# Kernel tuning notes

Hardware: AMD Instinct MI355X
Metric: run time of the kernel (lower is better)

## Reference

```python
import jax, jax.numpy as jnp
import numpy as np

N_NODES = 100000
N_EDGES = 1600000
N_GRAPHS = 512
NODE_DIM = 64   # len(node_indices)
GRAPH_DIM = 16  # len(graph_indices) == graph_channels
HIDDEN = 128
OUT = 8


def setup_inputs() -> dict:
    key = jax.random.key(0)
    ks = jax.random.split(key, 12)
    x = jax.random.normal(ks[0], (N_NODES, NODE_DIM + GRAPH_DIM), dtype=jnp.float32)
    edge_index = jax.random.randint(ks[1], (2, N_EDGES), 0, N_NODES, dtype=jnp.int64)
    batch = jnp.sort(jax.random.randint(ks[2], (N_NODES,), 0, N_GRAPHS, dtype=jnp.int64))
    def lin(k, fan_in, fan_out):
        lim = 1.0 / np.sqrt(fan_in)
        return jax.random.uniform(k, (fan_in, fan_out), jnp.float32, -lim, lim)
    return {
        "x": x, "edge_index": edge_index, "batch": batch,
        "W1": lin(ks[3], NODE_DIM, HIDDEN), "b1": jnp.zeros((HIDDEN,), jnp.float32),
        "W2": lin(ks[4], HIDDEN, HIDDEN),   "b2": jnp.zeros((HIDDEN,), jnp.float32),
        "Wm1": lin(ks[5], HIDDEN + GRAPH_DIM, HIDDEN), "bm1": jnp.zeros((HIDDEN,), jnp.float32),
        "Wm2": lin(ks[6], HIDDEN, OUT), "bm2": jnp.zeros((OUT,), jnp.float32),
    }


def _gcn_conv(h_in, src, dst, W, b):
    # PyG GCNConv: h = X W; out = D^{-1/2}(A+I)D^{-1/2} h + b, deg over A+I.
    h = h_in @ W                                        # [N, H]
    deg = jnp.zeros((N_NODES,), h.dtype).at[dst].add(1.0) + 1.0  # +1 self loop
    dinv = jax.lax.rsqrt(deg)                           # [N]
    norm = dinv[src] * dinv[dst]                        # [E]
    out = jnp.zeros_like(h).at[dst].add(norm[:, None] * h[src])
    out = out + (dinv * dinv)[:, None] * h              # self-loop term
    return out + b


def _mean_pool(v, batch):
    cnt = jax.ops.segment_sum(jnp.ones((v.shape[0],), v.dtype), batch, num_segments=N_GRAPHS)
    s = jax.ops.segment_sum(v, batch, num_segments=N_GRAPHS)
    return s / jnp.maximum(cnt, 1.0)[:, None]


def reference(x, edge_index, batch, W1, b1, W2, b2, Wm1, bm1, Wm2, bm2):
    src, dst = edge_index[0], edge_index[1]
    node_t = x[:, :NODE_DIM]                 # node_indices slice
    graph_t = _mean_pool(x[:, NODE_DIM:], batch)  # graph_indices slice, pooled [G, 16]
    h = _gcn_conv(node_t, src, dst, W1, b1)
    h = jax.nn.relu(h)                       # dropout is identity in eval mode
    h = _gcn_conv(h, src, dst, W2, b2)
    g = _mean_pool(h, batch)                 # [G, H]
    g = jnp.concatenate([g, graph_t], axis=1)
    g = jax.nn.relu(g @ Wm1 + bm1)
    return g @ Wm2 + bm2                     # [G, OUT]
```

## Files before the change

### kernel.cpp

```cpp
#include <hip/hip_runtime.h>
#include <hip/hip_bf16.h>

#define N_NODES 100000
#define N_EDGES 1600000
#define N_GRAPHS 512
#define NODE_DIM 64
#define GRAPH_DIM 16
#define HIDDEN 128
#define OUT_DIM 8

#define NBUCKETS 391
#define BIN_CAP 8192
#define EPB 4096

__device__ __forceinline__ float bflo(unsigned u) { return __uint_as_float(u << 16); }
__device__ __forceinline__ float bfhi(unsigned u) { return __uint_as_float(u & 0xffff0000u); }


__global__ __launch_bounds__(256) void k_binplace(const int* __restrict__ src,
                                                  const int* __restrict__ dst,
                                                  int* __restrict__ gcur,
                                                  unsigned* __restrict__ bin) {
    __shared__ int cnt[NBUCKETS];
    __shared__ int base[NBUCKETS];
    int t = threadIdx.x;
    for (int i = t; i < NBUCKETS; i += 256) cnt[i] = 0;
    __syncthreads();
    int e0 = blockIdx.x * EPB;
#pragma unroll
    for (int k = 0; k < EPB / 256; k++) {
        int e = e0 + k * 256 + t;
        if (e < N_EDGES) atomicAdd(&cnt[dst[e] >> 8], 1);
    }
    __syncthreads();
    for (int i = t; i < NBUCKETS; i += 256) {
        int c = cnt[i];
        base[i] = (c > 0) ? atomicAdd(&gcur[i], c) : 0;
        cnt[i] = 0;
    }
    __syncthreads();
#pragma unroll
    for (int k = 0; k < EPB / 256; k++) {
        int e = e0 + k * 256 + t;
        if (e < N_EDGES) {
            int d = dst[e];
            int b = d >> 8;
            int p = atomicAdd(&cnt[b], 1);
            bin[(size_t)b * BIN_CAP + base[b] + p] = ((unsigned)src[e] << 8) | (unsigned)(d & 255);
        }
    }
}


__global__ __launch_bounds__(256) void k_degBf(const int* __restrict__ gcur,
                                               const unsigned* __restrict__ bin,
                                               int* __restrict__ degcnt,
                                               float* __restrict__ dinv,
                                               int* __restrict__ bsum) {
    __shared__ int cnt[256];
    int b = blockIdx.x, t = threadIdx.x;
    cnt[t] = 0;
    __syncthreads();
    int n = gcur[b];
    const unsigned* seg = bin + (size_t)b * BIN_CAP;
    for (int i = t; i < n; i += 256) atomicAdd(&cnt[seg[i] & 255u], 1);
    __syncthreads();
    int c = cnt[t];
    int node = b * 256 + t;
    if (node < N_NODES) {
        degcnt[node] = c;
        dinv[node] = rsqrtf((float)c + 1.0f);
    }
    __syncthreads();
    for (int o = 128; o > 0; o >>= 1) {
        if (t < o) cnt[t] += cnt[t + o];
        __syncthreads();
    }
    if (t == 0) bsum[b] = cnt[0];
}


__global__ __launch_bounds__(512) void k_scanb(const int* __restrict__ bsum,
                                               int* __restrict__ bofs) {
    __shared__ int s[512];
    int t = threadIdx.x;
    int v = (t < NBUCKETS) ? bsum[t] : 0;
    s[t] = v;
    __syncthreads();
    for (int o = 1; o < 512; o <<= 1) {
        int u = (t >= o) ? s[t - o] : 0;
        __syncthreads();
        s[t] += u;
        __syncthreads();
    }
    if (t < NBUCKETS) bofs[t] = s[t] - v;
}


__global__ __launch_bounds__(256) void k_rowfill(const int* __restrict__ degcnt,
                                                 const int* __restrict__ bofs,
                                                 const int* __restrict__ gcur,
                                                 const unsigned* __restrict__ bin,
                                                 const float* __restrict__ dinv,
                                                 int* __restrict__ row_start,
                                                 int2* __restrict__ csre,
                                                 float* __restrict__ gt_sum) {
    __shared__ int sc[256];
    __shared__ int rsl[256];
    __shared__ int cnt[256];
    __shared__ float dl[256];
    int b = blockIdx.x, t = threadIdx.x;
    if (b < 32) gt_sum[b * 256 + t] = 0.0f;
    int node = b * 256 + t;
    int v = (node < N_NODES) ? degcnt[node] : 0;
    sc[t] = v;
    __syncthreads();
    for (int o = 1; o < 256; o <<= 1) {
        int u = (t >= o) ? sc[t - o] : 0;
        __syncthreads();
        sc[t] += u;
        __syncthreads();
    }
    int rs = bofs[b] + sc[t] - v;
    if (node < N_NODES) row_start[node] = rs;
    rsl[t] = rs;
    cnt[t] = 0;
    dl[t] = rsqrtf((float)v + 1.0f);
    __syncthreads();
    int n = gcur[b];
    const unsigned* seg = bin + (size_t)b * BIN_CAP;
    for (int i = t; i < n; i += 256) {
        unsigned e = seg[i];
        int dlidx = (int)(e & 255u);
        int s = (int)(e >> 8);
        int pos = rsl[dlidx] + atomicAdd(&cnt[dlidx], 1);
        csre[pos] = make_int2(s, __float_as_int(dinv[s] * dl[dlidx]));
    }
}


__global__ __launch_bounds__(256) void k_packstat(const float* __restrict__ x,
                                                  const int* __restrict__ batch,
                                                  ushort* __restrict__ xb,
                                                  float* __restrict__ gt_sum) {
    int t = threadIdx.x;
    int i0 = blockIdx.x * 64;
    for (int idx = t; idx < 64 * 32; idx += 256) {
        int node = i0 + (idx >> 5);
        if (node < N_NODES) {
            int c2 = idx & 31;
            float2 v = *(const float2*)&x[(size_t)node * 80 + c2 * 2];
            __hip_bfloat16 lo = __float2bfloat16(v.x);
            __hip_bfloat16 hi = __float2bfloat16(v.y);
            ushort2 pv = make_ushort2(*(ushort*)&lo, *(ushort*)&hi);
            ((ushort2*)xb)[(size_t)node * 32 + c2] = pv;
        }
    }
    int c = t & 15, sub = t >> 4;
    int iend = min(i0 + 64, N_NODES);
    float acc = 0.0f;
    int g = -1;
    for (int i = i0 + sub; i < iend; i += 16) {
        int bi = batch[i];
        if (bi != g) {
            if (g >= 0) atomicAdd(&gt_sum[g * GRAPH_DIM + c], acc);
            acc = 0.0f; g = bi;
        }
        acc += x[(size_t)i * 80 + NODE_DIM + c];
    }
    if (g >= 0) atomicAdd(&gt_sum[g * GRAPH_DIM + c], acc);
}


#define LDX(s_) __uint_as_float((unsigned)xb[(size_t)(s_)*64 + lane] << 16)

__global__ __launch_bounds__(256) void k_conv1(const int2* __restrict__ csre,
                                               const int* __restrict__ row_start,
                                               const float* __restrict__ dinv,
                                               const ushort* __restrict__ xb,
                                               const float* __restrict__ W,
                                               const float* __restrict__ bias,
                                               ushort* __restrict__ C,
                                               float* __restrict__ gsum2) {
    __shared__ float zs[8][64];
    int t = threadIdx.x;
    if (blockIdx.x < 256) gsum2[blockIdx.x * 256 + t] = 0.0f;
    int w = t >> 6, lane = t & 63;
    int nA = blockIdx.x * 8 + w * 2;
    int nB = nA + 1;
    int rsA = row_start[nA], reA = (nA == N_NODES - 1) ? N_EDGES : row_start[nA + 1];
    int rsB = row_start[nB], reB = (nB == N_NODES - 1) ? N_EDGES : row_start[nB + 1];
    float aA0 = 0.f, aA1 = 0.f, aA2 = 0.f, aA3 = 0.f;
    float aB0 = 0.f, aB1 = 0.f, aB2 = 0.f, aB3 = 0.f;
    int kA = rsA, kB = rsB;
    while (kA + 4 <= reA && kB + 4 <= reB) {
        int2 eA0 = csre[kA], eA1 = csre[kA + 1], eA2 = csre[kA + 2], eA3 = csre[kA + 3];
        int2 eB0 = csre[kB], eB1 = csre[kB + 1], eB2 = csre[kB + 2], eB3 = csre[kB + 3];
        float vA0 = LDX(eA0.x), vA1 = LDX(eA1.x), vA2 = LDX(eA2.x), vA3 = LDX(eA3.x);
        float vB0 = LDX(eB0.x), vB1 = LDX(eB1.x), vB2 = LDX(eB2.x), vB3 = LDX(eB3.x);
        aA0 += __int_as_float(eA0.y) * vA0; aA1 += __int_as_float(eA1.y) * vA1;
        aA2 += __int_as_float(eA2.y) * vA2; aA3 += __int_as_float(eA3.y) * vA3;
        aB0 += __int_as_float(eB0.y) * vB0; aB1 += __int_as_float(eB1.y) * vB1;
        aB2 += __int_as_float(eB2.y) * vB2; aB3 += __int_as_float(eB3.y) * vB3;
        kA += 4; kB += 4;
    }
    while (kA + 4 <= reA) {
        int2 e0 = csre[kA], e1 = csre[kA + 1], e2 = csre[kA + 2], e3 = csre[kA + 3];
        float v0 = LDX(e0.x), v1 = LDX(e1.x), v2 = LDX(e2.x), v3 = LDX(e3.x);
        aA0 += __int_as_float(e0.y) * v0; aA1 += __int_as_float(e1.y) * v1;
        aA2 += __int_as_float(e2.y) * v2; aA3 += __int_as_float(e3.y) * v3;
        kA += 4;
    }
    while (kB + 4 <= reB) {
        int2 e0 = csre[kB], e1 = csre[kB + 1], e2 = csre[kB + 2], e3 = csre[kB + 3];
        float v0 = LDX(e0.x), v1 = LDX(e1.x), v2 = LDX(e2.x), v3 = LDX(e3.x);
        aB0 += __int_as_float(e0.y) * v0; aB1 += __int_as_float(e1.y) * v1;
        aB2 += __int_as_float(e2.y) * v2; aB3 += __int_as_float(e3.y) * v3;
        kB += 4;
    }
    while (kA < reA && kB < reB) {
        int2 eA = csre[kA]; int2 eB = csre[kB];
        aA0 += __int_as_float(eA.y) * LDX(eA.x);
        aB0 += __int_as_float(eB.y) * LDX(eB.x);
        kA++; kB++;
    }
    while (kA < reA) { int2 e = csre[kA]; aA0 += __int_as_float(e.y) * LDX(e.x); kA++; }
    while (kB < reB) { int2 e = csre[kB]; aB0 += __int_as_float(e.y) * LDX(e.x); kB++; }
    float dA = dinv[nA], dB = dinv[nB];
    zs[w * 2][lane]     = aA0 + aA1 + aA2 + aA3 + dA * dA * LDX(nA);
    zs[w * 2 + 1][lane] = aB0 + aB1 + aB2 + aB3 + dB * dB * LDX(nB);
    __syncthreads();
    if (t < 128) {
        int j = t;
        float acc[8];
#pragma unroll
        for (int m = 0; m < 8; m++) acc[m] = 0.0f;
        for (int k = 0; k < 64; k++) {
            float wv = W[k * 128 + j];
#pragma unroll
            for (int m = 0; m < 8; m++) acc[m] += zs[m][k] * wv;
        }
        float b = bias[j];
        size_t row0 = (size_t)blockIdx.x * 8;
#pragma unroll
        for (int m = 0; m < 8; m++) {
            float v = fmaxf(acc[m] + b, 0.0f);
            __hip_bfloat16 hv = __float2bfloat16(v);
            C[(row0 + m) * 128 + j] = *(ushort*)&hv;
        }
    }
}


__global__ __launch_bounds__(256) void k_gather2(const int2* __restrict__ csre,
                                                 const int* __restrict__ row_start,
                                                 const float* __restrict__ dinv,
                                                 const unsigned* __restrict__ h,
                                                 const int* __restrict__ batch,
                                                 float* __restrict__ gsum2) {
    __shared__ float2 red[8][64];
    int w = threadIdx.x >> 6, lane = threadIdx.x & 63;
    int nA = blockIdx.x * 8 + w * 2;
    int nB = nA + 1;
    int rsA = row_start[nA], reA = (nA == N_NODES - 1) ? N_EDGES : row_start[nA + 1];
    int rsB = row_start[nB], reB = (nB == N_NODES - 1) ? N_EDGES : row_start[nB + 1];
    float2 aA0 = {0.f,0.f}, aA1 = {0.f,0.f}, aA2 = {0.f,0.f}, aA3 = {0.f,0.f};
    float2 aB0 = {0.f,0.f}, aB1 = {0.f,0.f}, aB2 = {0.f,0.f}, aB3 = {0.f,0.f};
    int kA = rsA, kB = rsB;
#define FMA2(acc_, wbits_, u_) { float w_ = __int_as_float(wbits_); \
                             acc_.x += w_ * bflo(u_); acc_.y += w_ * bfhi(u_); }
    while (kA + 4 <= reA && kB + 4 <= reB) {
        int2 eA0 = csre[kA], eA1 = csre[kA + 1], eA2 = csre[kA + 2], eA3 = csre[kA + 3];
        int2 eB0 = csre[kB], eB1 = csre[kB + 1], eB2 = csre[kB + 2], eB3 = csre[kB + 3];
        unsigned uA0 = h[(size_t)eA0.x * 64 + lane], uA1 = h[(size_t)eA1.x * 64 + lane];
        unsigned uA2 = h[(size_t)eA2.x * 64 + lane], uA3 = h[(size_t)eA3.x * 64 + lane];
        unsigned uB0 = h[(size_t)eB0.x * 64 + lane], uB1 = h[(size_t)eB1.x * 64 + lane];
        unsigned uB2 = h[(size_t)eB2.x * 64 + lane], uB3 = h[(size_t)eB3.x * 64 + lane];
        FMA2(aA0, eA0.y, uA0); FMA2(aA1, eA1.y, uA1); FMA2(aA2, eA2.y, uA2); FMA2(aA3, eA3.y, uA3);
        FMA2(aB0, eB0.y, uB0); FMA2(aB1, eB1.y, uB1); FMA2(aB2, eB2.y, uB2); FMA2(aB3, eB3.y, uB3);
        kA += 4; kB += 4;
    }
    while (kA + 4 <= reA) {
        int2 e0 = csre[kA], e1 = csre[kA + 1], e2 = csre[kA + 2], e3 = csre[kA + 3];
        unsigned u0 = h[(size_t)e0.x * 64 + lane], u1 = h[(size_t)e1.x * 64 + lane];
        unsigned u2 = h[(size_t)e2.x * 64 + lane], u3 = h[(size_t)e3.x * 64 + lane];
        FMA2(aA0, e0.y, u0); FMA2(aA1, e1.y, u1); FMA2(aA2, e2.y, u2); FMA2(aA3, e3.y, u3);
        kA += 4;
    }
    while (kB + 4 <= reB) {
        int2 e0 = csre[kB], e1 = csre[kB + 1], e2 = csre[kB + 2], e3 = csre[kB + 3];
        unsigned u0 = h[(size_t)e0.x * 64 + lane], u1 = h[(size_t)e1.x * 64 + lane];
        unsigned u2 = h[(size_t)e2.x * 64 + lane], u3 = h[(size_t)e3.x * 64 + lane];
        FMA2(aB0, e0.y, u0); FMA2(aB1, e1.y, u1); FMA2(aB2, e2.y, u2); FMA2(aB3, e3.y, u3);
        kB += 4;
    }
    while (kA < reA && kB < reB) {
        int2 eA = csre[kA]; int2 eB = csre[kB];
        unsigned uA = h[(size_t)eA.x * 64 + lane], uB = h[(size_t)eB.x * 64 + lane];
        FMA2(aA0, eA.y, uA); FMA2(aB0, eB.y, uB);
        kA++; kB++;
    }
    while (kA < reA) {
        int2 e = csre[kA]; unsigned u = h[(size_t)e.x * 64 + lane];
        FMA2(aA0, e.y, u); kA++;
    }
    while (kB < reB) {
        int2 e = csre[kB]; unsigned u = h[(size_t)e.x * 64 + lane];
        FMA2(aB0, e.y, u); kB++;
    }
#undef FMA2
    float dA = dinv[nA], dB = dinv[nB];
    unsigned usA = h[(size_t)nA * 64 + lane];
    unsigned usB = h[(size_t)nB * 64 + lane];
    float2 rA, rB;
    rA.x = aA0.x + aA1.x + aA2.x + aA3.x + dA * dA * bflo(usA);
    rA.y = aA0.y + aA1.y + aA2.y + aA3.y + dA * dA * bfhi(usA);
    rB.x = aB0.x + aB1.x + aB2.x + aB3.x + dB * dB * bflo(usB);
    rB.y = aB0.y + aB1.y + aB2.y + aB3.y + dB * dB * bfhi(usB);
    red[w * 2][lane] = rA;
    red[w * 2 + 1][lane] = rB;
    __syncthreads();
    int g0 = batch[blockIdx.x * 8];
    int g7 = batch[blockIdx.x * 8 + 7];
    if (g0 == g7) {
        if (w == 0) {
            float sx = 0.f, sy = 0.f;
#pragma unroll
            for (int q = 0; q < 8; q++) { sx += red[q][lane].x; sy += red[q][lane].y; }
            atomicAdd(&gsum2[g0 * 128 + 2 * lane], sx);
            atomicAdd(&gsum2[g0 * 128 + 2 * lane + 1], sy);
        }
    } else {
        int gA = batch[nA], gB = batch[nB];
        atomicAdd(&gsum2[gA * 128 + 2 * lane], rA.x);
        atomicAdd(&gsum2[gA * 128 + 2 * lane + 1], rA.y);
        atomicAdd(&gsum2[gB * 128 + 2 * lane], rB.x);
        atomicAdd(&gsum2[gB * 128 + 2 * lane + 1], rB.y);
    }
}


__global__ __launch_bounds__(128) void k_mlp(const float* __restrict__ gsum2,
                                             const float* __restrict__ gt_sum,
                                             const int* __restrict__ batch,
                                             const float* __restrict__ W2,
                                             const float* __restrict__ b2,
                                             const float* __restrict__ Wm1,
                                             const float* __restrict__ bm1,
                                             const float* __restrict__ Wm2,
                                             const float* __restrict__ bm2,
                                             float* __restrict__ out) {
    __shared__ float srow[HIDDEN];
    __shared__ float g144[HIDDEN + GRAPH_DIM];
    __shared__ float sm[HIDDEN];
    __shared__ int cnt_sh;
    int b = blockIdx.x;
    int j = threadIdx.x;
    float raw = gsum2[b * 128 + j];
    float gtraw = (j < GRAPH_DIM) ? gt_sum[b * GRAPH_DIM + j] : 0.0f;
    if (j == 0) {
        int lo = 0, hi = N_NODES;
        while (lo < hi) { int m = (lo + hi) >> 1; if (batch[m] < b) lo = m + 1; else hi = m; }
        int a = lo;
        lo = 0; hi = N_NODES;
        while (lo < hi) { int m = (lo + hi) >> 1; if (batch[m] < b + 1) lo = m + 1; else hi = m; }
        cnt_sh = lo - a;
    }
    __syncthreads();
    float inv = 1.0f / fmaxf((float)cnt_sh, 1.0f);
    srow[j] = raw * inv;
    if (j < GRAPH_DIM) g144[128 + j] = gtraw * inv;
    __syncthreads();
    float z = b2[j];
    for (int k = 0; k < 128; k++) z += srow[k] * W2[k * 128 + j];
    g144[j] = z;
    __syncthreads();
    float acc = bm1[j];
    for (int k = 0; k < HIDDEN + GRAPH_DIM; k++) acc += g144[k] * Wm1[k * 128 + j];
    sm[j] = fmaxf(acc, 0.0f);
    __syncthreads();
    if (j < OUT_DIM) {
        float o = bm2[j];
        for (int k = 0; k < 128; k++) o += sm[k] * Wm2[k * OUT_DIM + j];
        out[b * OUT_DIM + j] = o;
    }
}

extern "C" void kernel_launch(void* const* d_in, const int* in_sizes, int n_in,
                              void* d_out, int out_size, void* d_ws, size_t ws_size,
                              hipStream_t stream) {
    const float* x    = (const float*)d_in[0];
    const int*   edge = (const int*)d_in[1];
    const int*   src  = edge;
    const int*   dst  = edge + N_EDGES;
    const int*   batch= (const int*)d_in[2];
    const float* W1   = (const float*)d_in[3];
    const float* b1   = (const float*)d_in[4];
    const float* W2   = (const float*)d_in[5];
    const float* b2   = (const float*)d_in[6];
    const float* Wm1  = (const float*)d_in[7];
    const float* bm1  = (const float*)d_in[8];
    const float* Wm2  = (const float*)d_in[9];
    const float* bm2  = (const float*)d_in[10];
    float* out = (float*)d_out;

    char* ws = (char*)d_ws;
    char* p = ws;
    unsigned* bin   = (unsigned*)p;  p += (size_t)NBUCKETS * BIN_CAP * 4;
    int2*  csre     = (int2*)p;      p += (size_t)N_EDGES * 8;
    ushort* h1b     = (ushort*)p;    p += (size_t)N_NODES * 128 * 2;
    ushort* xb      = (ushort*)p;    p += (size_t)N_NODES * 64 * 2;
    int*   degcnt   = (int*)p;       p += (size_t)NBUCKETS * 256 * 4;
    int*   row_start= (int*)p;       p += (size_t)N_NODES * 4;
    float* dinv     = (float*)p;     p += (size_t)N_NODES * 4;
    int*   gcur     = (int*)p;       p += (size_t)NBUCKETS * 4;
    int*   bsum     = (int*)p;       p += 512 * 4;
    int*   bofs     = (int*)p;       p += 512 * 4;
    float* gt_sum   = (float*)p;     p += (size_t)N_GRAPHS * GRAPH_DIM * 4;
    float* gsum2    = (float*)p;     p += (size_t)N_GRAPHS * 128 * 4;

    hipMemsetAsync(gcur, 0, (size_t)NBUCKETS * 4, stream);

    k_binplace<<<(N_EDGES + EPB - 1) / EPB, 256, 0, stream>>>(src, dst, gcur, bin);
    k_degBf<<<NBUCKETS, 256, 0, stream>>>(gcur, bin, degcnt, dinv, bsum);
    k_scanb<<<1, 512, 0, stream>>>(bsum, bofs);
    k_rowfill<<<NBUCKETS, 256, 0, stream>>>(degcnt, bofs, gcur, bin, dinv, row_start, csre, gt_sum);

    k_packstat<<<(N_NODES + 63) / 64, 256, 0, stream>>>(x, batch, xb, gt_sum);

    k_conv1<<<N_NODES / 8, 256, 0, stream>>>(csre, row_start, dinv, xb, W1, b1, h1b, gsum2);

    k_gather2<<<N_NODES / 8, 256, 0, stream>>>(csre, row_start, dinv,
                                               (const unsigned*)h1b, batch, gsum2);

    k_mlp<<<N_GRAPHS, 128, 0, stream>>>(gsum2, gt_sum, batch, W2, b2, Wm1, bm1, Wm2, bm2, out);
}
```

Measured before the change: 248.2 us.

## Halve bucket size, fuse bucket scan into degree kernel, pad CSR for unrolled gathers

Buckets now hold 128 destination nodes instead of 256, which doubles the number of blocks used for binning, degree counting and row fill. The separate bucket-sum scan kernel is removed: block 0 of the degree kernel scans the global bucket counts directly. The CSR gets padding entries and a sentinel row_start, so both gather kernels can run a single 8-wide unrolled loop with masked weights instead of several remainder loops. This cuts one launch and the tail-loop branching, at the cost of some wasted loads on short rows. Block 0 reads gcur, which is final after the previous kernel, so the fused scan is correct.

```diff
diff --git a/kernel.cpp b/kernel.cpp
--- a/kernel.cpp
+++ b/kernel.cpp
@@ -9,8 +9,9 @@
 #define HIDDEN 128
 #define OUT_DIM 8
 
-#define NBUCKETS 391
-#define BIN_CAP 8192
+#define NBUCKETS 782
+#define BNODES 128
+#define BIN_CAP 4096
 #define EPB 4096
 
 __device__ __forceinline__ float bflo(unsigned u) { return __uint_as_float(u << 16); }
@@ -30,7 +31,7 @@
 #pragma unroll
     for (int k = 0; k < EPB / 256; k++) {
         int e = e0 + k * 256 + t;
-        if (e < N_EDGES) atomicAdd(&cnt[dst[e] >> 8], 1);
+        if (e < N_EDGES) atomicAdd(&cnt[dst[e] >> 7], 1);
     }
     __syncthreads();
     for (int i = t; i < NBUCKETS; i += 256) {
@@ -44,56 +45,55 @@
         int e = e0 + k * 256 + t;
         if (e < N_EDGES) {
             int d = dst[e];
-            int b = d >> 8;
+            int b = d >> 7;
             int p = atomicAdd(&cnt[b], 1);
-            bin[(size_t)b * BIN_CAP + base[b] + p] = ((unsigned)src[e] << 8) | (unsigned)(d & 255);
-        }
-    }
-}
-
-
-__global__ __launch_bounds__(256) void k_degBf(const int* __restrict__ gcur,
-                                               const unsigned* __restrict__ bin,
-                                               int* __restrict__ degcnt,
-                                               float* __restrict__ dinv,
-                                               int* __restrict__ bsum) {
-    __shared__ int cnt[256];
+            bin[(size_t)b * BIN_CAP + base[b] + p] = ((unsigned)src[e] << 7) | (unsigned)(d & 127);
+        }
+    }
+}
+
+
+__global__ __launch_bounds__(256) void k_degscan(const int* __restrict__ gcur,
+                                                 const unsigned* __restrict__ bin,
+                                                 int* __restrict__ degcnt,
+                                                 float* __restrict__ dinv,
+                                                 int* __restrict__ bofs) {
+    __shared__ int cnt[BNODES];
     int b = blockIdx.x, t = threadIdx.x;
-    cnt[t] = 0;
+    if (t < BNODES) cnt[t] = 0;
     __syncthreads();
     int n = gcur[b];
     const unsigned* seg = bin + (size_t)b * BIN_CAP;
-    for (int i = t; i < n; i += 256) atomicAdd(&cnt[seg[i] & 255u], 1);
-    __syncthreads();
-    int c = cnt[t];
-    int node = b * 256 + t;
-    if (node < N_NODES) {
+    for (int i = t; i < n; i += 256) atomicAdd(&cnt[seg[i] & 127u], 1);
+    __syncthreads();
+    int node = b * BNODES + t;
+    if (t < BNODES && node < N_NODES) {
+        int c = cnt[t];
         degcnt[node] = c;
         dinv[node] = rsqrtf((float)c + 1.0f);
     }
-    __syncthreads();
-    for (int o = 128; o > 0; o >>= 1) {
-        if (t < o) cnt[t] += cnt[t + o];
+    if (b == 0) {
+        __shared__ int ls[256];
+        int i0 = 4 * t;
+        int c0 = (i0 + 0 < NBUCKETS) ? gcur[i0 + 0] : 0;
+        int c1 = (i0 + 1 < NBUCKETS) ? gcur[i0 + 1] : 0;
+        int c2 = (i0 + 2 < NBUCKETS) ? gcur[i0 + 2] : 0;
+        int c3 = (i0 + 3 < NBUCKETS) ? gcur[i0 + 3] : 0;
+        int s = c0 + c1 + c2 + c3;
+        ls[t] = s;
         __syncthreads();
-    }
-    if (t == 0) bsum[b] = cnt[0];
-}
-
-
-__global__ __launch_bounds__(512) void k_scanb(const int* __restrict__ bsum,
-                                               int* __restrict__ bofs) {
-    __shared__ int s[512];
-    int t = threadIdx.x;
-    int v = (t < NBUCKETS) ? bsum[t] : 0;
-    s[t] = v;
-    __syncthreads();
-    for (int o = 1; o < 512; o <<= 1) {
-        int u = (t >= o) ? s[t - o] : 0;
-        __syncthreads();
-        s[t] += u;
-        __syncthreads();
-    }
-    if (t < NBUCKETS) bofs[t] = s[t] - v;
+        for (int o = 1; o < 256; o <<= 1) {
+            int u = (t >= o) ? ls[t - o] : 0;
+            __syncthreads();
+            ls[t] += u;
+            __syncthreads();
+        }
+        int run = ls[t] - s;
+        if (i0 + 0 < NBUCKETS) bofs[i0 + 0] = run; run += c0;
+        if (i0 + 1 < NBUCKETS) bofs[i0 + 1] = run; run += c1;
+        if (i0 + 2 < NBUCKETS) bofs[i0 + 2] = run; run += c2;
+        if (i0 + 3 < NBUCKETS) bofs[i0 + 3] = run;
+    }
 }
 
 
@@ -105,36 +105,46 @@
                                                  int* __restrict__ row_start,
                                                  int2* __restrict__ csre,
                                                  float* __restrict__ gt_sum) {
-    __shared__ int sc[256];
-    __shared__ int rsl[256];
-    __shared__ int cnt[256];
-    __shared__ float dl[256];
+    __shared__ int sc[BNODES];
+    __shared__ int rsl[BNODES];
+    __shared__ int cnt[BNODES];
+    __shared__ float dl[BNODES];
     int b = blockIdx.x, t = threadIdx.x;
     if (b < 32) gt_sum[b * 256 + t] = 0.0f;
-    int node = b * 256 + t;
-    int v = (node < N_NODES) ? degcnt[node] : 0;
-    sc[t] = v;
-    __syncthreads();
-    for (int o = 1; o < 256; o <<= 1) {
-        int u = (t >= o) ? sc[t - o] : 0;
+    int node = b * BNODES + t;
+    int v = 0;
+    if (t < BNODES) {
+        v = (node < N_NODES) ? degcnt[node] : 0;
+        sc[t] = v;
+    }
+    __syncthreads();
+    for (int o = 1; o < BNODES; o <<= 1) {
+        int u = 0;
+        if (t < BNODES && t >= o) u = sc[t - o];
         __syncthreads();
-        sc[t] += u;
+        if (t < BNODES) sc[t] += u;
         __syncthreads();
     }
-    int rs = bofs[b] + sc[t] - v;
-    if (node < N_NODES) row_start[node] = rs;
-    rsl[t] = rs;
-    cnt[t] = 0;
-    dl[t] = rsqrtf((float)v + 1.0f);
+    if (t < BNODES) {
+        int rs = bofs[b] + sc[t] - v;
+        if (node < N_NODES) row_start[node] = rs;
+        rsl[t] = rs;
+        cnt[t] = 0;
+        dl[t] = rsqrtf((float)v + 1.0f);
+    }
     __syncthreads();
     int n = gcur[b];
     const unsigned* seg = bin + (size_t)b * BIN_CAP;
     for (int i = t; i < n; i += 256) {
         unsigned e = seg[i];
-        int dlidx = (int)(e & 255u);
-        int s = (int)(e >> 8);
+        int dlidx = (int)(e & 127u);
+        int s = (int)(e >> 7);
         int pos = rsl[dlidx] + atomicAdd(&cnt[dlidx], 1);
         csre[pos] = make_int2(s, __float_as_int(dinv[s] * dl[dlidx]));
+    }
+    if (b == NBUCKETS - 1) {
+        if (t < 8) csre[N_EDGES + t] = make_int2(0, 0);
+        if (t == 8) row_start[N_NODES] = N_EDGES;
     }
 }
 
@@ -185,50 +195,52 @@
     __shared__ float zs[8][64];
     int t = threadIdx.x;
     if (blockIdx.x < 256) gsum2[blockIdx.x * 256 + t] = 0.0f;
-    int w = t >> 6, lane = t & 63;
-    int nA = blockIdx.x * 8 + w * 2;
+    int wv = t >> 6, lane = t & 63;
+    int nA = blockIdx.x * 8 + wv * 2;
     int nB = nA + 1;
-    int rsA = row_start[nA], reA = (nA == N_NODES - 1) ? N_EDGES : row_start[nA + 1];
-    int rsB = row_start[nB], reB = (nB == N_NODES - 1) ? N_EDGES : row_start[nB + 1];
+    int kA = row_start[nA], reA = row_start[nA + 1];
+    int kB = reA,           reB = row_start[nB + 1];
     float aA0 = 0.f, aA1 = 0.f, aA2 = 0.f, aA3 = 0.f;
     float aB0 = 0.f, aB1 = 0.f, aB2 = 0.f, aB3 = 0.f;
-    int kA = rsA, kB = rsB;
-    while (kA + 4 <= reA && kB + 4 <= reB) {
-        int2 eA0 = csre[kA], eA1 = csre[kA + 1], eA2 = csre[kA + 2], eA3 = csre[kA + 3];
-        int2 eB0 = csre[kB], eB1 = csre[kB + 1], eB2 = csre[kB + 2], eB3 = csre[kB + 3];
-        float vA0 = LDX(eA0.x), vA1 = LDX(eA1.x), vA2 = LDX(eA2.x), vA3 = LDX(eA3.x);
-        float vB0 = LDX(eB0.x), vB1 = LDX(eB1.x), vB2 = LDX(eB2.x), vB3 = LDX(eB3.x);
-        aA0 += __int_as_float(eA0.y) * vA0; aA1 += __int_as_float(eA1.y) * vA1;
-        aA2 += __int_as_float(eA2.y) * vA2; aA3 += __int_as_float(eA3.y) * vA3;
-        aB0 += __int_as_float(eB0.y) * vB0; aB1 += __int_as_float(eB1.y) * vB1;
-        aB2 += __int_as_float(eB2.y) * vB2; aB3 += __int_as_float(eB3.y) * vB3;
-        kA += 4; kB += 4;
-    }
-    while (kA + 4 <= reA) {
-        int2 e0 = csre[kA], e1 = csre[kA + 1], e2 = csre[kA + 2], e3 = csre[kA + 3];
-        float v0 = LDX(e0.x), v1 = LDX(e1.x), v2 = LDX(e2.x), v3 = LDX(e3.x);
-        aA0 += __int_as_float(e0.y) * v0; aA1 += __int_as_float(e1.y) * v1;
-        aA2 += __int_as_float(e2.y) * v2; aA3 += __int_as_float(e3.y) * v3;
-        kA += 4;
-    }
-    while (kB + 4 <= reB) {
-        int2 e0 = csre[kB], e1 = csre[kB + 1], e2 = csre[kB + 2], e3 = csre[kB + 3];
-        float v0 = LDX(e0.x), v1 = LDX(e1.x), v2 = LDX(e2.x), v3 = LDX(e3.x);
-        aB0 += __int_as_float(e0.y) * v0; aB1 += __int_as_float(e1.y) * v1;
-        aB2 += __int_as_float(e2.y) * v2; aB3 += __int_as_float(e3.y) * v3;
-        kB += 4;
-    }
-    while (kA < reA && kB < reB) {
-        int2 eA = csre[kA]; int2 eB = csre[kB];
-        aA0 += __int_as_float(eA.y) * LDX(eA.x);
-        aB0 += __int_as_float(eB.y) * LDX(eB.x);
-        kA++; kB++;
-    }
-    while (kA < reA) { int2 e = csre[kA]; aA0 += __int_as_float(e.y) * LDX(e.x); kA++; }
-    while (kB < reB) { int2 e = csre[kB]; aB0 += __int_as_float(e.y) * LDX(e.x); kB++; }
+    while (kA < reA || kB < reB) {
+        if (kA < reA) {
+            int2 e0 = csre[kA],     e1 = csre[kA + 1], e2 = csre[kA + 2], e3 = csre[kA + 3];
+            int2 e4 = csre[kA + 4], e5 = csre[kA + 5], e6 = csre[kA + 6], e7 = csre[kA + 7];
+            float w0 = (kA + 0 < reA) ? __int_as_float(e0.y) : 0.f;
+            float w1 = (kA + 1 < reA) ? __int_as_float(e1.y) : 0.f;
+            float w2 = (kA + 2 < reA) ? __int_as_float(e2.y) : 0.f;
+            float w3 = (kA + 3 < reA) ? __int_as_float(e3.y) : 0.f;
+            float w4 = (kA + 4 < reA) ? __int_as_float(e4.y) : 0.f;
+            float w5 = (kA + 5 < reA) ? __int_as_float(e5.y) : 0.f;
+            float w6 = (kA + 6 < reA) ? __int_as_float(e6.y) : 0.f;
+            float w7 = (kA + 7 < reA) ? __int_as_float(e7.y) : 0.f;
+            float v0 = LDX(e0.x), v1 = LDX(e1.x), v2 = LDX(e2.x), v3 = LDX(e3.x);
+            float v4 = LDX(e4.x), v5 = LDX(e5.x), v6 = LDX(e6.x), v7 = LDX(e7.x);
+            aA0 += w0 * v0; aA1 += w1 * v1; aA2 += w2 * v2; aA3 += w3 * v3;
+            aA0 += w4 * v4; aA1 += w5 * v5; aA2 += w6 * v6; aA3 += w7 * v7;
+            kA += 8;
+        }
+        if (kB < reB) {
+            int2 e0 = csre[kB],     e1 = csre[kB + 1], e2 = csre[kB + 2], e3 = csre[kB + 3];
+            int2 e4 = csre[kB + 4], e5 = csre[kB + 5], e6 = csre[kB + 6], e7 = csre[kB + 7];
+            float w0 = (kB + 0 < reB) ? __int_as_float(e0.y) : 0.f;
+            float w1 = (kB + 1 < reB) ? __int_as_float(e1.y) : 0.f;
+            float w2 = (kB + 2 < reB) ? __int_as_float(e2.y) : 0.f;
+            float w3 = (kB + 3 < reB) ? __int_as_float(e3.y) : 0.f;
+            float w4 = (kB + 4 < reB) ? __int_as_float(e4.y) : 0.f;
+            float w5 = (kB + 5 < reB) ? __int_as_float(e5.y) : 0.f;
+            float w6 = (kB + 6 < reB) ? __int_as_float(e6.y) : 0.f;
+            float w7 = (kB + 7 < reB) ? __int_as_float(e7.y) : 0.f;
+            float v0 = LDX(e0.x), v1 = LDX(e1.x), v2 = LDX(e2.x), v3 = LDX(e3.x);
+            float v4 = LDX(e4.x), v5 = LDX(e5.x), v6 = LDX(e6.x), v7 = LDX(e7.x);
+            aB0 += w0 * v0; aB1 += w1 * v1; aB2 += w2 * v2; aB3 += w3 * v3;
+            aB0 += w4 * v4; aB1 += w5 * v5; aB2 += w6 * v6; aB3 += w7 * v7;
+            kB += 8;
+        }
+    }
     float dA = dinv[nA], dB = dinv[nB];
-    zs[w * 2][lane]     = aA0 + aA1 + aA2 + aA3 + dA * dA * LDX(nA);
-    zs[w * 2 + 1][lane] = aB0 + aB1 + aB2 + aB3 + dB * dB * LDX(nB);
+    zs[wv * 2][lane]     = aA0 + aA1 + aA2 + aA3 + dA * dA * LDX(nA);
+    zs[wv * 2 + 1][lane] = aB0 + aB1 + aB2 + aB3 + dB * dB * LDX(nB);
     __syncthreads();
     if (t < 128) {
         int j = t;
@@ -236,9 +248,9 @@
 #pragma unroll
         for (int m = 0; m < 8; m++) acc[m] = 0.0f;
         for (int k = 0; k < 64; k++) {
-            float wv = W[k * 128 + j];
-#pragma unroll
-            for (int m = 0; m < 8; m++) acc[m] += zs[m][k] * wv;
+            float wv2 = W[k * 128 + j];
+#pragma unroll
+            for (int m = 0; m < 8; m++) acc[m] += zs[m][k] * wv2;
         }
         float b = bias[j];
         size_t row0 = (size_t)blockIdx.x * 8;
@@ -262,51 +274,50 @@
     int w = threadIdx.x >> 6, lane = threadIdx.x & 63;
     int nA = blockIdx.x * 8 + w * 2;
     int nB = nA + 1;
-    int rsA = row_start[nA], reA = (nA == N_NODES - 1) ? N_EDGES : row_start[nA + 1];
-    int rsB = row_start[nB], reB = (nB == N_NODES - 1) ? N_EDGES : row_start[nB + 1];
+    int kA = row_start[nA], reA = row_start[nA + 1];
+    int kB = reA,           reB = row_start[nB + 1];
     float2 aA0 = {0.f,0.f}, aA1 = {0.f,0.f}, aA2 = {0.f,0.f}, aA3 = {0.f,0.f};
     float2 aB0 = {0.f,0.f}, aB1 = {0.f,0.f}, aB2 = {0.f,0.f}, aB3 = {0.f,0.f};
-    int kA = rsA, kB = rsB;
-#define FMA2(acc_, wbits_, u_) { float w_ = __int_as_float(wbits_); \
-                             acc_.x += w_ * bflo(u_); acc_.y += w_ * bfhi(u_); }
-    while (kA + 4 <= reA && kB + 4 <= reB) {
-        int2 eA0 = csre[kA], eA1 = csre[kA + 1], eA2 = csre[kA + 2], eA3 = csre[kA + 3];
-        int2 eB0 = csre[kB], eB1 = csre[kB + 1], eB2 = csre[kB + 2], eB3 = csre[kB + 3];
-        unsigned uA0 = h[(size_t)eA0.x * 64 + lane], uA1 = h[(size_t)eA1.x * 64 + lane];
-        unsigned uA2 = h[(size_t)eA2.x * 64 + lane], uA3 = h[(size_t)eA3.x * 64 + lane];
-        unsigned uB0 = h[(size_t)eB0.x * 64 + lane], uB1 = h[(size_t)eB1.x * 64 + lane];
-        unsigned uB2 = h[(size_t)eB2.x * 64 + lane], uB3 = h[(size_t)eB3.x * 64 + lane];
-        FMA2(aA0, eA0.y, uA0); FMA2(aA1, eA1.y, uA1); FMA2(aA2, eA2.y, uA2); FMA2(aA3, eA3.y, uA3);
-        FMA2(aB0, eB0.y, uB0); FMA2(aB1, eB1.y, uB1); FMA2(aB2, eB2.y, uB2); FMA2(aB3, eB3.y, uB3);
-        kA += 4; kB += 4;
-    }
-    while (kA + 4 <= reA) {
-        int2 e0 = csre[kA], e1 = csre[kA + 1], e2 = csre[kA + 2], e3 = csre[kA + 3];
-        unsigned u0 = h[(size_t)e0.x * 64 + lane], u1 = h[(size_t)e1.x * 64 + lane];
-        unsigned u2 = h[(size_t)e2.x * 64 + lane], u3 = h[(size_t)e3.x * 64 + lane];
-        FMA2(aA0, e0.y, u0); FMA2(aA1, e1.y, u1); FMA2(aA2, e2.y, u2); FMA2(aA3, e3.y, u3);
-        kA += 4;
-    }
-    while (kB + 4 <= reB) {
-        int2 e0 = csre[kB], e1 = csre[kB + 1], e2 = csre[kB + 2], e3 = csre[kB + 3];
-        unsigned u0 = h[(size_t)e0.x * 64 + lane], u1 = h[(size_t)e1.x * 64 + lane];
-        unsigned u2 = h[(size_t)e2.x * 64 + lane], u3 = h[(size_t)e3.x * 64 + lane];
-        FMA2(aB0, e0.y, u0); FMA2(aB1, e1.y, u1); FMA2(aB2, e2.y, u2); FMA2(aB3, e3.y, u3);
-        kB += 4;
-    }
-    while (kA < reA && kB < reB) {
-        int2 eA = csre[kA]; int2 eB = csre[kB];
-        unsigned uA = h[(size_t)eA.x * 64 + lane], uB = h[(size_t)eB.x * 64 + lane];
-        FMA2(aA0, eA.y, uA); FMA2(aB0, eB.y, uB);
-        kA++; kB++;
-    }
-    while (kA < reA) {
-        int2 e = csre[kA]; unsigned u = h[(size_t)e.x * 64 + lane];
-        FMA2(aA0, e.y, u); kA++;
-    }
-    while (kB < reB) {
-        int2 e = csre[kB]; unsigned u = h[(size_t)e.x * 64 + lane];
-        FMA2(aB0, e.y, u); kB++;
+#define FMA2(acc_, w_, u_) { acc_.x += (w_) * bflo(u_); acc_.y += (w_) * bfhi(u_); }
+    while (kA < reA || kB < reB) {
+        if (kA < reA) {
+            int2 e0 = csre[kA],     e1 = csre[kA + 1], e2 = csre[kA + 2], e3 = csre[kA + 3];
+            int2 e4 = csre[kA + 4], e5 = csre[kA + 5], e6 = csre[kA + 6], e7 = csre[kA + 7];
+            float w0 = (kA + 0 < reA) ? __int_as_float(e0.y) : 0.f;
+            float w1 = (kA + 1 < reA) ? __int_as_float(e1.y) : 0.f;
+            float w2 = (kA + 2 < reA) ? __int_as_float(e2.y) : 0.f;
+            float w3 = (kA + 3 < reA) ? __int_as_float(e3.y) : 0.f;
+            float w4 = (kA + 4 < reA) ? __int_as_float(e4.y) : 0.f;
+            float w5 = (kA + 5 < reA) ? __int_as_float(e5.y) : 0.f;
+            float w6 = (kA + 6 < reA) ? __int_as_float(e6.y) : 0.f;
+            float w7 = (kA + 7 < reA) ? __int_as_float(e7.y) : 0.f;
+            unsigned u0 = h[(size_t)e0.x * 64 + lane], u1 = h[(size_t)e1.x * 64 + lane];
+            unsigned u2 = h[(size_t)e2.x * 64 + lane], u3 = h[(size_t)e3.x * 64 + lane];
+            unsigned u4 = h[(size_t)e4.x * 64 + lane], u5 = h[(size_t)e5.x * 64 + lane];
+            unsigned u6 = h[(size_t)e6.x * 64 + lane], u7 = h[(size_t)e7.x * 64 + lane];
+            FMA2(aA0, w0, u0); FMA2(aA1, w1, u1); FMA2(aA2, w2, u2); FMA2(aA3, w3, u3);
+            FMA2(aA0, w4, u4); FMA2(aA1, w5, u5); FMA2(aA2, w6, u6); FMA2(aA3, w7, u7);
+            kA += 8;
+        }
+        if (kB < reB) {
+            int2 e0 = csre[kB],     e1 = csre[kB + 1], e2 = csre[kB + 2], e3 = csre[kB + 3];
+            int2 e4 = csre[kB + 4], e5 = csre[kB + 5], e6 = csre[kB + 6], e7 = csre[kB + 7];
+            float w0 = (kB + 0 < reB) ? __int_as_float(e0.y) : 0.f;
+            float w1 = (kB + 1 < reB) ? __int_as_float(e1.y) : 0.f;
+            float w2 = (kB + 2 < reB) ? __int_as_float(e2.y) : 0.f;
+            float w3 = (kB + 3 < reB) ? __int_as_float(e3.y) : 0.f;
+            float w4 = (kB + 4 < reB) ? __int_as_float(e4.y) : 0.f;
+            float w5 = (kB + 5 < reB) ? __int_as_float(e5.y) : 0.f;
+            float w6 = (kB + 6 < reB) ? __int_as_float(e6.y) : 0.f;
+            float w7 = (kB + 7 < reB) ? __int_as_float(e7.y) : 0.f;
+            unsigned u0 = h[(size_t)e0.x * 64 + lane], u1 = h[(size_t)e1.x * 64 + lane];
+            unsigned u2 = h[(size_t)e2.x * 64 + lane], u3 = h[(size_t)e3.x * 64 + lane];
+            unsigned u4 = h[(size_t)e4.x * 64 + lane], u5 = h[(size_t)e5.x * 64 + lane];
+            unsigned u6 = h[(size_t)e6.x * 64 + lane], u7 = h[(size_t)e7.x * 64 + lane];
+            FMA2(aB0, w0, u0); FMA2(aB1, w1, u1); FMA2(aB2, w2, u2); FMA2(aB3, w3, u3);
+            FMA2(aB0, w4, u4); FMA2(aB1, w5, u5); FMA2(aB2, w6, u6); FMA2(aB3, w7, u7);
+            kB += 8;
+        }
     }
 #undef FMA2
     float dA = dinv[nA], dB = dinv[nB];
@@ -407,23 +418,21 @@
     char* ws = (char*)d_ws;
     char* p = ws;
     unsigned* bin   = (unsigned*)p;  p += (size_t)NBUCKETS * BIN_CAP * 4;
-    int2*  csre     = (int2*)p;      p += (size_t)N_EDGES * 8;
+    int2*  csre     = (int2*)p;      p += ((size_t)N_EDGES + 8) * 8;
     ushort* h1b     = (ushort*)p;    p += (size_t)N_NODES * 128 * 2;
     ushort* xb      = (ushort*)p;    p += (size_t)N_NODES * 64 * 2;
-    int*   degcnt   = (int*)p;       p += (size_t)NBUCKETS * 256 * 4;
-    int*   row_start= (int*)p;       p += (size_t)N_NODES * 4;
+    int*   degcnt   = (int*)p;       p += (size_t)NBUCKETS * BNODES * 4;
+    int*   row_start= (int*)p;       p += ((size_t)N_NODES + 1) * 4;
     float* dinv     = (float*)p;     p += (size_t)N_NODES * 4;
     int*   gcur     = (int*)p;       p += (size_t)NBUCKETS * 4;
-    int*   bsum     = (int*)p;       p += 512 * 4;
-    int*   bofs     = (int*)p;       p += 512 * 4;
+    int*   bofs     = (int*)p;       p += (size_t)NBUCKETS * 4;
     float* gt_sum   = (float*)p;     p += (size_t)N_GRAPHS * GRAPH_DIM * 4;
     float* gsum2    = (float*)p;     p += (size_t)N_GRAPHS * 128 * 4;
 
     hipMemsetAsync(gcur, 0, (size_t)NBUCKETS * 4, stream);
 
     k_binplace<<<(N_EDGES + EPB - 1) / EPB, 256, 0, stream>>>(src, dst, gcur, bin);
-    k_degBf<<<NBUCKETS, 256, 0, stream>>>(gcur, bin, degcnt, dinv, bsum);
-    k_scanb<<<1, 512, 0, stream>>>(bsum, bofs);
+    k_degscan<<<NBUCKETS, 256, 0, stream>>>(gcur, bin, degcnt, dinv, bofs);
     k_rowfill<<<NBUCKETS, 256, 0, stream>>>(degcnt, bofs, gcur, bin, dinv, row_start, csre, gt_sum);
 
     k_packstat<<<(N_NODES + 63) / 64, 256, 0, stream>>>(x, batch, xb, gt_sum);
```

After: 290.5 us. 1.17x slower.

## Split hidden features into two channel planes and gather each plane separately

Applied to the files above, without the earlier changes.

conv1 now writes its 128-channel bf16 output as two planes of 64 channels, [N,64] each, instead of one interleaved [N,128] array. The second gather launches twice as many blocks, and each block aggregates one plane for 8 nodes, interleaving the two phases so that nearby blocks share a plane. The aim is to halve the bytes fetched per neighbour per lane and make the gathered working set smaller and more cache-friendly. The cost is reading the CSR edge lists twice and issuing twice as many blocks and atomics per channel group. It also reuses row end A as row start B, which assumes consecutive rows.

```diff
diff --git a/kernel.cpp b/kernel.cpp
--- a/kernel.cpp
+++ b/kernel.cpp
@@ -188,11 +188,12 @@
     int w = t >> 6, lane = t & 63;
     int nA = blockIdx.x * 8 + w * 2;
     int nB = nA + 1;
-    int rsA = row_start[nA], reA = (nA == N_NODES - 1) ? N_EDGES : row_start[nA + 1];
-    int rsB = row_start[nB], reB = (nB == N_NODES - 1) ? N_EDGES : row_start[nB + 1];
+    int kA = row_start[nA];
+    int reA = (nA == N_NODES - 1) ? N_EDGES : row_start[nA + 1];
+    int kB = reA;
+    int reB = (nB == N_NODES - 1) ? N_EDGES : row_start[nB + 1];
     float aA0 = 0.f, aA1 = 0.f, aA2 = 0.f, aA3 = 0.f;
     float aB0 = 0.f, aB1 = 0.f, aB2 = 0.f, aB3 = 0.f;
-    int kA = rsA, kB = rsB;
     while (kA + 4 <= reA && kB + 4 <= reB) {
         int2 eA0 = csre[kA], eA1 = csre[kA + 1], eA2 = csre[kA + 2], eA3 = csre[kA + 3];
         int2 eB0 = csre[kB], eB1 = csre[kB + 1], eB2 = csre[kB + 2], eB3 = csre[kB + 3];
@@ -242,100 +243,94 @@
         }
         float b = bias[j];
         size_t row0 = (size_t)blockIdx.x * 8;
+        ushort* Cp = C + ((j >> 6) ? (size_t)N_NODES * 64 : 0);
+        int jc = j & 63;
 #pragma unroll
         for (int m = 0; m < 8; m++) {
             float v = fmaxf(acc[m] + b, 0.0f);
             __hip_bfloat16 hv = __float2bfloat16(v);
-            C[(row0 + m) * 128 + j] = *(ushort*)&hv;
-        }
-    }
-}
-
-
-__global__ __launch_bounds__(256) void k_gather2(const int2* __restrict__ csre,
-                                                 const int* __restrict__ row_start,
-                                                 const float* __restrict__ dinv,
-                                                 const unsigned* __restrict__ h,
-                                                 const int* __restrict__ batch,
-                                                 float* __restrict__ gsum2) {
-    __shared__ float2 red[8][64];
+            Cp[(row0 + m) * 64 + jc] = *(ushort*)&hv;
+        }
+    }
+}
+
+
+#define LDH(s_) __uint_as_float((unsigned)hp[(size_t)(s_)*64 + lane] << 16)
+
+__global__ __launch_bounds__(256) void k_gather2s(const int2* __restrict__ csre,
+                                                  const int* __restrict__ row_start,
+                                                  const float* __restrict__ dinv,
+                                                  const ushort* __restrict__ h1planes,
+                                                  const int* __restrict__ batch,
+                                                  float* __restrict__ gsum2) {
+    __shared__ float red[8][64];
+    int b = blockIdx.x;
+    int r = b & 7;
+    int phase = r >> 2;
+    int nb = (b >> 3) * 4 + (r & 3);
+    const ushort* hp = h1planes + (size_t)phase * N_NODES * 64;
     int w = threadIdx.x >> 6, lane = threadIdx.x & 63;
-    int nA = blockIdx.x * 8 + w * 2;
+    int nA = nb * 8 + w * 2;
     int nB = nA + 1;
-    int rsA = row_start[nA], reA = (nA == N_NODES - 1) ? N_EDGES : row_start[nA + 1];
-    int rsB = row_start[nB], reB = (nB == N_NODES - 1) ? N_EDGES : row_start[nB + 1];
-    float2 aA0 = {0.f,0.f}, aA1 = {0.f,0.f}, aA2 = {0.f,0.f}, aA3 = {0.f,0.f};
-    float2 aB0 = {0.f,0.f}, aB1 = {0.f,0.f}, aB2 = {0.f,0.f}, aB3 = {0.f,0.f};
-    int kA = rsA, kB = rsB;
-#define FMA2(acc_, wbits_, u_) { float w_ = __int_as_float(wbits_); \
-                             acc_.x += w_ * bflo(u_); acc_.y += w_ * bfhi(u_); }
+    int kA = row_start[nA];
+    int reA = (nA == N_NODES - 1) ? N_EDGES : row_start[nA + 1];
+    int kB = reA;
+    int reB = (nB == N_NODES - 1) ? N_EDGES : row_start[nB + 1];
+    float aA0 = 0.f, aA1 = 0.f, aA2 = 0.f, aA3 = 0.f;
+    float aB0 = 0.f, aB1 = 0.f, aB2 = 0.f, aB3 = 0.f;
     while (kA + 4 <= reA && kB + 4 <= reB) {
         int2 eA0 = csre[kA], eA1 = csre[kA + 1], eA2 = csre[kA + 2], eA3 = csre[kA + 3];
         int2 eB0 = csre[kB], eB1 = csre[kB + 1], eB2 = csre[kB + 2], eB3 = csre[kB + 3];
-        unsigned uA0 = h[(size_t)eA0.x * 64 + lane], uA1 = h[(size_t)eA1.x * 64 + lane];
-        unsigned uA2 = h[(size_t)eA2.x * 64 + lane], uA3 = h[(size_t)eA3.x * 64 + lane];
-        unsigned uB0 = h[(size_t)eB0.x * 64 + lane], uB1 = h[(size_t)eB1.x * 64 + lane];
-        unsigned uB2 = h[(size_t)eB2.x * 64 + lane], uB3 = h[(size_t)eB3.x * 64 + lane];
-        FMA2(aA0, eA0.y, uA0); FMA2(aA1, eA1.y, uA1); FMA2(aA2, eA2.y, uA2); FMA2(aA3, eA3.y, uA3);
-        FMA2(aB0, eB0.y, uB0); FMA2(aB1, eB1.y, uB1); FMA2(aB2, eB2.y, uB2); FMA2(aB3, eB3.y, uB3);
+        float vA0 = LDH(eA0.x), vA1 = LDH(eA1.x), vA2 = LDH(eA2.x), vA3 = LDH(eA3.x);
+        float vB0 = LDH(eB0.x), vB1 = LDH(eB1.x), vB2 = LDH(eB2.x), vB3 = LDH(eB3.x);
+        aA0 += __int_as_float(eA0.y) * vA0; aA1 += __int_as_float(eA1.y) * vA1;
+        aA2 += __int_as_float(eA2.y) * vA2; aA3 += __int_as_float(eA3.y) * vA3;
+        aB0 += __int_as_float(eB0.y) * vB0; aB1 += __int_as_float(eB1.y) * vB1;
+        aB2 += __int_as_float(eB2.y) * vB2; aB3 += __int_as_float(eB3.y) * vB3;
         kA += 4; kB += 4;
     }
     while (kA + 4 <= reA) {
         int2 e0 = csre[kA], e1 = csre[kA + 1], e2 = csre[kA + 2], e3 = csre[kA + 3];
-        unsigned u0 = h[(size_t)e0.x * 64 + lane], u1 = h[(size_t)e1.x * 64 + lane];
-        unsigned u2 = h[(size_t)e2.x * 64 + lane], u3 = h[(size_t)e3.x * 64 + lane];
-        FMA2(aA0, e0.y, u0); FMA2(aA1, e1.y, u1); FMA2(aA2, e2.y, u2); FMA2(aA3, e3.y, u3);
+        float v0 = LDH(e0.x), v1 = LDH(e1.x), v2 = LDH(e2.x), v3 = LDH(e3.x);
+        aA0 += __int_as_float(e0.y) * v0; aA1 += __int_as_float(e1.y) * v1;
+        aA2 += __int_as_float(e2.y) * v2; aA3 += __int_as_float(e3.y) * v3;
         kA += 4;
     }
     while (kB + 4 <= reB) {
         int2 e0 = csre[kB], e1 = csre[kB + 1], e2 = csre[kB + 2], e3 = csre[kB + 3];
-        unsigned u0 = h[(size_t)e0.x * 64 + lane], u1 = h[(size_t)e1.x * 64 + lane];
-        unsigned u2 = h[(size_t)e2.x * 64 + lane], u3 = h[(size_t)e3.x * 64 + lane];
-        FMA2(aB0, e0.y, u0); FMA2(aB1, e1.y, u1); FMA2(aB2, e2.y, u2); FMA2(aB3, e3.y, u3);
+        float v0 = LDH(e0.x), v1 = LDH(e1.x), v2 = LDH(e2.x), v3 = LDH(e3.x);
+        aB0 += __int_as_float(e0.y) * v0; aB1 += __int_as_float(e1.y) * v1;
+        aB2 += __int_as_float(e2.y) * v2; aB3 += __int_as_float(e3.y) * v3;
         kB += 4;
     }
     while (kA < reA && kB < reB) {
         int2 eA = csre[kA]; int2 eB = csre[kB];
-        unsigned uA = h[(size_t)eA.x * 64 + lane], uB = h[(size_t)eB.x * 64 + lane];
-        FMA2(aA0, eA.y, uA); FMA2(aB0, eB.y, uB);
+        aA0 += __int_as_float(eA.y) * LDH(eA.x);
+        aB0 += __int_as_float(eB.y) * LDH(eB.x);
         kA++; kB++;
     }
-    while (kA < reA) {
-        int2 e = csre[kA]; unsigned u = h[(size_t)e.x * 64 + lane];
-        FMA2(aA0, e.y, u); kA++;
-    }
-    while (kB < reB) {
-        int2 e = csre[kB]; unsigned u = h[(size_t)e.x * 64 + lane];
-        FMA2(aB0, e.y, u); kB++;
-    }
-#undef FMA2
+    while (kA < reA) { int2 e = csre[kA]; aA0 += __int_as_float(e.y) * LDH(e.x); kA++; }
+    while (kB < reB) { int2 e = csre[kB]; aB0 += __int_as_float(e.y) * LDH(e.x); kB++; }
     float dA = dinv[nA], dB = dinv[nB];
-    unsigned usA = h[(size_t)nA * 64 + lane];
-    unsigned usB = h[(size_t)nB * 64 + lane];
-    float2 rA, rB;
-    rA.x = aA0.x + aA1.x + aA2.x + aA3.x + dA * dA * bflo(usA);
-    rA.y = aA0.y + aA1.y + aA2.y + aA3.y + dA * dA * bfhi(usA);
-    rB.x = aB0.x + aB1.x + aB2.x + aB3.x + dB * dB * bflo(usB);
-    rB.y = aB0.y + aB1.y + aB2.y + aB3.y + dB * dB * bfhi(usB);
+    float rA = aA0 + aA1 + aA2 + aA3 + dA * dA * LDH(nA);
+    float rB = aB0 + aB1 + aB2 + aB3 + dB * dB * LDH(nB);
     red[w * 2][lane] = rA;
     red[w * 2 + 1][lane] = rB;
     __syncthreads();
-    int g0 = batch[blockIdx.x * 8];
-    int g7 = batch[blockIdx.x * 8 + 7];
+    int g0 = batch[nb * 8];
+    int g7 = batch[nb * 8 + 7];
+    int chofs = phase * 64 + lane;
     if (g0 == g7) {
         if (w == 0) {
-            float sx = 0.f, sy = 0.f;
-#pragma unroll
-            for (int q = 0; q < 8; q++) { sx += red[q][lane].x; sy += red[q][lane].y; }
-            atomicAdd(&gsum2[g0 * 128 + 2 * lane], sx);
-            atomicAdd(&gsum2[g0 * 128 + 2 * lane + 1], sy);
+            float s = 0.f;
+#pragma unroll
+            for (int q = 0; q < 8; q++) s += red[q][lane];
+            atomicAdd(&gsum2[g0 * 128 + chofs], s);
         }
     } else {
         int gA = batch[nA], gB = batch[nB];
-        atomicAdd(&gsum2[gA * 128 + 2 * lane], rA.x);
-        atomicAdd(&gsum2[gA * 128 + 2 * lane + 1], rA.y);
-        atomicAdd(&gsum2[gB * 128 + 2 * lane], rB.x);
-        atomicAdd(&gsum2[gB * 128 + 2 * lane + 1], rB.y);
+        atomicAdd(&gsum2[gA * 128 + chofs], rA);
+        atomicAdd(&gsum2[gB * 128 + chofs], rB);
     }
 }
 
@@ -407,11 +402,11 @@
     char* ws = (char*)d_ws;
     char* p = ws;
     unsigned* bin   = (unsigned*)p;  p += (size_t)NBUCKETS * BIN_CAP * 4;
-    int2*  csre     = (int2*)p;      p += (size_t)N_EDGES * 8;
+    int2*  csre     = (int2*)p;      p += ((size_t)N_EDGES + 8) * 8;
     ushort* h1b     = (ushort*)p;    p += (size_t)N_NODES * 128 * 2;
     ushort* xb      = (ushort*)p;    p += (size_t)N_NODES * 64 * 2;
     int*   degcnt   = (int*)p;       p += (size_t)NBUCKETS * 256 * 4;
-    int*   row_start= (int*)p;       p += (size_t)N_NODES * 4;
+    int*   row_start= (int*)p;       p += ((size_t)N_NODES + 1) * 4;
     float* dinv     = (float*)p;     p += (size_t)N_NODES * 4;
     int*   gcur     = (int*)p;       p += (size_t)NBUCKETS * 4;
     int*   bsum     = (int*)p;       p += 512 * 4;
@@ -430,8 +425,7 @@
 
     k_conv1<<<N_NODES / 8, 256, 0, stream>>>(csre, row_start, dinv, xb, W1, b1, h1b, gsum2);
 
-    k_gather2<<<N_NODES / 8, 256, 0, stream>>>(csre, row_start, dinv,
-                                               (const unsigned*)h1b, batch, gsum2);
+    k_gather2s<<<25000, 256, 0, stream>>>(csre, row_start, dinv, h1b, batch, gsum2);
 
     k_mlp<<<N_GRAPHS, 128, 0, stream>>>(gsum2, gt_sum, batch, W2, b2, Wm1, bm1, Wm2, bm2, out);
 }
```

Result: slower. 289.1 us (+16.5%).
